# Kernel optimization log

Measured on AMD Instinct MI355X. Metric: run time of the kernel, lower is better.

Reference implementation:

```python
import jax, jax.numpy as jnp
import numpy as np
from jax import lax

STRIDE = 2
PADDING = 2
KERNEL = 5


def _conv_transpose3d(x, weight, bias):
    # weight: [C_in, C_out, kd, kh, kw] (PyTorch ConvTranspose3d layout)
    # Equivalent dense conv: flip kernel spatially, swap in/out channels,
    # lhs_dilation=stride, symmetric padding = dilation*(k-1) - padding.
    w_t = jnp.flip(weight, axis=(2, 3, 4)).transpose(1, 0, 2, 3, 4)  # [C_out, C_in, k,k,k]
    pad = KERNEL - 1 - PADDING  # = 2
    y = lax.conv_general_dilated(
        x, w_t,
        window_strides=(1, 1, 1),
        padding=[(pad, pad)] * 3,
        lhs_dilation=(STRIDE, STRIDE, STRIDE),
        dimension_numbers=("NCDHW", "OIDHW", "NCDHW"),
    )
    return y + bias[None, :, None, None, None]


def _maxpool3d(y, k):
    # PyTorch MaxPool3d(kernel=k) -> stride=k, no padding, floor mode == VALID
    win = (1, 1, k, k, k)
    return lax.reduce_window(y, -jnp.inf, lax.max, win, win, "VALID")


def setup_inputs() -> dict:
    key = jax.random.key(0)
    k1, k2, k3 = jax.random.split(key, 3)
    x = jax.random.normal(k1, (16, 32, 16, 32, 32), dtype=jnp.float32)
    weight = jax.random.normal(k2, (32, 64, 5, 5, 5), dtype=jnp.float32) * 0.05
    bias = jax.random.normal(k3, (64,), dtype=jnp.float32) * 0.05
    return {"x": x, "weight": weight, "bias": bias}


def reference(x, weight, bias):
    y = _conv_transpose3d(x, weight, bias)     # [16, 64, 31, 63, 63]
    y = _maxpool3d(y, 2)                       # [16, 64, 15, 31, 31]
    y = _maxpool3d(y, 3)                       # [16, 64, 5, 10, 10]
    return jnp.sum(y, axis=1, keepdims=True)   # [16, 1, 5, 10, 10]
```

## Files before the change

kernel.cpp:

```cpp
#include <hip/hip_runtime.h>
#include <hip/hip_bf16.h>
#include <math.h>

typedef short bf16x8 __attribute__((ext_vector_type(8)));
typedef float f32x4 __attribute__((ext_vector_type(4)));

constexpr int CIN = 32, COUT = 64, D = 16, H = 32, W = 32;

constexpr size_t WS_XT_OFF = 1u << 20;
constexpr size_t WS_NEED   = WS_XT_OFF + 33554432u;

static __device__ const unsigned char IT_CODE[24] = {
    0, 8, 16, 3,
    1, 9, 17, 11, 19, 7,
    2, 10, 18, 5, 13, 21, 15,
    4, 12, 20, 6, 14, 22, 23};
static __device__ const unsigned char IT_START[5] = {0, 4, 10, 17, 24};
static __device__ const unsigned char EPI_START[10] = {0, 1, 3, 5, 6, 7, 9, 11, 12, 13};
static __device__ const unsigned char EPI_CNT[10]   = {1, 2, 2, 1, 1, 2, 2, 1, 1, 2};

__global__ __launch_bounds__(1024) void prep_all(
    const float* __restrict__ x, const float* __restrict__ w,
    unsigned short* __restrict__ xT, unsigned short* __restrict__ wtp) {
    __shared__ float tile[4][32][33];
    int tid = threadIdx.x;
    if (blockIdx.x < 2048) {
        int sub = tid >> 8, t = tid & 255;
        int tileIdx = blockIdx.x * 4 + sub;
        int ih = tileIdx & 31, id = (tileIdx >> 5) & 15, n = tileIdx >> 9;
        int ci = t >> 3, iwq = t & 7;
        float4 v = ((const float4*)(x + ((((size_t)n * CIN + ci) * D + id) * H + ih) * W))[iwq];
        tile[sub][ci][iwq * 4 + 0] = v.x;
        tile[sub][ci][iwq * 4 + 1] = v.y;
        tile[sub][ci][iwq * 4 + 2] = v.z;
        tile[sub][ci][iwq * 4 + 3] = v.w;
        __syncthreads();
        int iw = t >> 3, ciq = t & 7;
        ushort4 o;
        {
            __hip_bfloat16 b0 = __float2bfloat16(tile[sub][ciq * 4 + 0][iw]);
            __hip_bfloat16 b1 = __float2bfloat16(tile[sub][ciq * 4 + 1][iw]);
            __hip_bfloat16 b2 = __float2bfloat16(tile[sub][ciq * 4 + 2][iw]);
            __hip_bfloat16 b3 = __float2bfloat16(tile[sub][ciq * 4 + 3][iw]);
            o.x = *reinterpret_cast<unsigned short*>(&b0);
            o.y = *reinterpret_cast<unsigned short*>(&b1);
            o.z = *reinterpret_cast<unsigned short*>(&b2);
            o.w = *reinterpret_cast<unsigned short*>(&b3);
        }
        ((ushort4*)(xT + ((((size_t)n * D + id) * H + ih) * W) * 32))[iw * 8 + ciq] = o;
    } else {
        int idx = (blockIdx.x - 2048) * 1024 + tid;
        int ci  = idx & 31;
        int co  = (idx >> 5) & 63;
        int tt  = idx >> 11;
        int t   = tt % 27, cls = tt / 27;
        int td = t / 9, th = (t / 3) % 3, tw = t % 3;
        int pd = (cls >> 2) & 1, ph = (cls >> 1) & 1, pw = cls & 1;
        int kd = pd + 2 * td, kh = ph + 2 * th, kw = pw + 2 * tw;
        float v = 0.f;
        if (kd < 5 && kh < 5 && kw < 5)
            v = w[(ci * COUT + co) * 125 + kd * 25 + kh * 5 + kw];
        __hip_bfloat16 b = __float2bfloat16(v);
        wtp[idx] = *reinterpret_cast<unsigned short*>(&b);
    }
}

__device__ __forceinline__ int lpA(int wrow, int quad) {
    return wrow * 64 + ((quad ^ ((wrow >> 1) & 3)) << 4);
}

__global__ __launch_bounds__(256, 3) void main_k(
    const unsigned short* __restrict__ wtp, const unsigned short* __restrict__ xT,
    const float* __restrict__ bias, float* __restrict__ out)
{
    __shared__ unsigned short Xs[25600];
    int bx = blockIdx.x;
    int h0 = bx % 10;
    int d0 = (bx / 10) % 5;
    int n  = bx / 50;
    int tid = threadIdx.x;

    int id0 = 3 * d0 - 1, ih0 = 3 * h0 - 1;
    for (int i = tid; i < 3200; i += 256) {
        int cb = i & 3, ww = (i >> 2) & 31, hl = (i >> 7) % 5, dd = i / 640;
        int id = id0 + dd, ih = ih0 + hl, iw = ww - 1;
        float4 v = {0.f, 0.f, 0.f, 0.f};
        if (id >= 0 && ih >= 0 && iw >= 0)
            v = ((const float4*)(xT + ((((size_t)n * D + id) * H + ih) * W + iw) * 32))[cb];
        ((float4*)Xs)[(i >> 2) * 4 + (cb ^ ((ww >> 1) & 3))] = v;
    }

    int lane = tid & 63, wv = tid >> 6;
    int l15 = lane & 15, quad = lane >> 4;
    int wv_s = __builtin_amdgcn_readfirstlane(wv);

    int laneB = l15 * 64 + quad * 16;
    int m1 = 16 + l15; if (m1 > 29) m1 = 29;
    int lp00 = lpA(l15 + 0, quad), lp01 = lpA(l15 + 1, quad), lp02 = lpA(l15 + 2, quad);
    int lp10 = lpA(m1 + 0, quad),  lp11 = lpA(m1 + 1, quad),  lp12 = lpA(m1 + 2, quad);

    f32x4 mx[2][4];
#pragma unroll
    for (int mt = 0; mt < 2; ++mt)
#pragma unroll
        for (int nt = 0; nt < 4; ++nt) mx[mt][nt] = (f32x4){-INFINITY, -INFINITY, -INFINITY, -INFINITY};

    __syncthreads();
    const char* xsb = (const char*)Xs;

    int it0 = IT_START[wv_s], it1 = IT_START[wv_s + 1];
#pragma unroll 1
    for (int ii = it0; ii < it1; ++ii) {
        int code  = __builtin_amdgcn_readfirstlane(IT_CODE[ii]);
        int cls   = code & 7;
        int alpha = code >> 3;
        int ntd = 3 - ((cls >> 2) & 1), nth = 3 - ((cls >> 1) & 1), ntw = 3 - (cls & 1);
        const char* tbb = (const char*)wtp + (size_t)cls * 27 * 4096 + laneB;

        f32x4 acc[3][2][4];
#pragma unroll
        for (int b = 0; b < 3; ++b)
#pragma unroll
            for (int mt = 0; mt < 2; ++mt)
#pragma unroll
                for (int nt = 0; nt < 4; ++nt) acc[b][mt][nt] = (f32x4){0.f, 0.f, 0.f, 0.f};

        const int T = ntd * nth * ntw;
        bf16x8 nb0 = *(const bf16x8*)(tbb);
        bf16x8 nb1 = *(const bf16x8*)(tbb + 1024);
        bf16x8 nb2 = *(const bf16x8*)(tbb + 2048);
        bf16x8 nb3 = *(const bf16x8*)(tbb + 3072);
        int ptd = 0, pth = 0, ptw = 0;
        int nQb = ((alpha + 2) * 5 + 2) * 2048;
        int nss = 2;

#pragma unroll 1
        for (int it = 0; it < T; ++it) {
            bf16x8 b0 = nb0, b1 = nb1, b2 = nb2, b3 = nb3;
            const int Qb = nQb, ss = nss;

            if (it + 1 < T) {
                ++ptw;
                if (ptw == ntw) { ptw = 0; ++pth; if (pth == nth) { pth = 0; ++ptd; } }
            }
            nQb = ((alpha + 2 - ptd) * 5 + (2 - pth)) * 2048;
            nss = 2 - ptw;
            const char* bq = tbb + (ptd * 9 + pth * 3 + ptw) * 4096;
            nb0 = *(const bf16x8*)(bq);
            nb1 = *(const bf16x8*)(bq + 1024);
            nb2 = *(const bf16x8*)(bq + 2048);
            nb3 = *(const bf16x8*)(bq + 3072);

            int lpa = ss == 0 ? lp00 : (ss == 1 ? lp01 : lp02);
            int lpb = ss == 0 ? lp10 : (ss == 1 ? lp11 : lp12);

#pragma unroll
            for (int beta = 0; beta < 3; ++beta) {
                const char* rb = xsb + Qb + beta * 2048;
                bf16x8 af0 = *(const bf16x8*)(rb + lpa);
                bf16x8 af1 = *(const bf16x8*)(rb + lpb);
                acc[beta][0][0] = __builtin_amdgcn_mfma_f32_16x16x32_bf16(af0, b0, acc[beta][0][0], 0, 0, 0);
                acc[beta][0][1] = __builtin_amdgcn_mfma_f32_16x16x32_bf16(af0, b1, acc[beta][0][1], 0, 0, 0);
                acc[beta][0][2] = __builtin_amdgcn_mfma_f32_16x16x32_bf16(af0, b2, acc[beta][0][2], 0, 0, 0);
                acc[beta][0][3] = __builtin_amdgcn_mfma_f32_16x16x32_bf16(af0, b3, acc[beta][0][3], 0, 0, 0);
                acc[beta][1][0] = __builtin_amdgcn_mfma_f32_16x16x32_bf16(af1, b0, acc[beta][1][0], 0, 0, 0);
                acc[beta][1][1] = __builtin_amdgcn_mfma_f32_16x16x32_bf16(af1, b1, acc[beta][1][1], 0, 0, 0);
                acc[beta][1][2] = __builtin_amdgcn_mfma_f32_16x16x32_bf16(af1, b2, acc[beta][1][2], 0, 0, 0);
                acc[beta][1][3] = __builtin_amdgcn_mfma_f32_16x16x32_bf16(af1, b3, acc[beta][1][3], 0, 0, 0);
            }
        }

#pragma unroll
        for (int mt = 0; mt < 2; ++mt)
#pragma unroll
            for (int nt = 0; nt < 4; ++nt)
#pragma unroll
                for (int r = 0; r < 4; ++r) {
                    float m = fmaxf(fmaxf(acc[0][mt][nt][r], acc[1][mt][nt][r]), acc[2][mt][nt][r]);
                    mx[mt][nt][r] = fmaxf(mx[mt][nt][r], m);
                }
    }

    __syncthreads();
    float* epi = (float*)Xs;
    int fsm0 = (0x3123 >> (quad * 4)) & 15;
    int fsm1 = (0x4312 >> (quad * 4)) & 15;
#pragma unroll
    for (int mt = 0; mt < 2; ++mt) {
        int fs = mt ? fsm1 : fsm0;
        int g  = mt * 4 + quad;
#pragma unroll
        for (int nt = 0; nt < 4; ++nt) {
            float a0 = mx[mt][nt][0], a1 = mx[mt][nt][1], a2 = mx[mt][nt][2], a3 = mx[mt][nt][3];
            float t01 = fmaxf(a0, a1), t012 = fmaxf(t01, a2), t0123 = fmaxf(t012, a3);
            float pA = fs == 1 ? a0 : (fs == 2 ? t01 : (fs == 3 ? t012 : t0123));
            float t23 = fmaxf(a2, a3), t123 = fmaxf(a1, t23);
            float pB = fs == 1 ? t123 : (fs == 2 ? t23 : (fs == 3 ? a3 : -INFINITY));
            epi[((wv * 8 + g) * 2 + 0) * 64 + nt * 16 + l15] = pA;
            epi[((wv * 8 + g) * 2 + 1) * 64 + nt * 16 + l15] = pB;
        }
    }
    __syncthreads();

    int elemBase = ((n * 5 + d0) * 10 + h0) * 10;
    float bco = bias[lane];
#pragma unroll 1
    for (int win = wv_s; win < 10; win += 4) {
        int st = EPI_START[win], cnt = EPI_CNT[win];
        float v = -INFINITY;
        for (int src = 0; src < 4; ++src)
            for (int e = st; e < st + cnt; ++e)
                v = fmaxf(v, epi[(src * 16 + e) * 64 + lane]);
        v += bco;
#pragma unroll
        for (int off = 32; off > 0; off >>= 1) v += __shfl_xor(v, off);
        if (lane == 0) out[elemBase + win] = v;
    }
}

__global__ __launch_bounds__(256) void fused_fallback(
    const float* __restrict__ x, const float* __restrict__ wsrc,
    const float* __restrict__ bias, float* __restrict__ out)
{
    __shared__ float xs[CIN * 125];
    __shared__ float wmax[4][64];
    const int b  = blockIdx.x;
    const int w0 = b % 10, h0 = (b / 10) % 10, d0 = (b / 100) % 5, n = b / 500;
    const int tid = threadIdx.x;
    const int id0 = 3 * d0 - 1, ih0 = 3 * h0 - 1, iw0 = 3 * w0 - 1;
    for (int e = tid; e < CIN * 125; e += 256) {
        int kk = e % 5, jj = (e / 5) % 5, ii = (e / 25) % 5, c = e / 125;
        int id = id0 + ii, ih = ih0 + jj, iw = iw0 + kk;
        float v = 0.f;
        if (id >= 0 && ih >= 0 && iw >= 0)
            v = x[(((n * CIN + c) * D + id) * H + ih) * W + iw];
        xs[e] = v;
    }
    __syncthreads();
    const int lane = tid & 63, wv = tid >> 6;
    float lmax = -INFINITY;
    for (int ccls = 0; ccls < 2; ++ccls) {
        const int cls = wv * 2 + ccls;
        const int pd = (cls >> 2) & 1, ph = (cls >> 1) & 1, pw = cls & 1;
        float acc[27];
#pragma unroll
        for (int i = 0; i < 27; ++i) acc[i] = 0.f;
        for (int ci = 0; ci < CIN; ++ci) {
            float wr[27];
#pragma unroll
            for (int t = 0; t < 27; ++t) {
                int td = t / 9, th = (t / 3) % 3, tw = t % 3;
                int kd = pd + 2 * td, kh = ph + 2 * th, kw = pw + 2 * tw;
                wr[t] = (kd < 5 && kh < 5 && kw < 5)
                          ? wsrc[((ci * 64 + lane) * 125) + kd * 25 + kh * 5 + kw] : 0.f;
            }
            const float* xb = xs + ci * 125;
#pragma unroll
            for (int td = 0; td < 3; ++td)
#pragma unroll
            for (int th = 0; th < 3; ++th)
#pragma unroll
            for (int tw = 0; tw < 3; ++tw) {
                const float wval = wr[(td * 3 + th) * 3 + tw];
#pragma unroll
                for (int a = 0; a < 3; ++a)
#pragma unroll
                for (int bb = 0; bb < 3; ++bb)
#pragma unroll
                for (int cc = 0; cc < 3; ++cc)
                    acc[(a * 3 + bb) * 3 + cc] +=
                        xb[(a + 2 - td) * 25 + (bb + 2 - th) * 5 + (cc + 2 - tw)] * wval;
            }
        }
#pragma unroll
        for (int i = 0; i < 27; ++i) lmax = fmaxf(lmax, acc[i]);
    }
    wmax[wv][lane] = lmax;
    __syncthreads();
    if (wv == 0) {
        float m = fmaxf(fmaxf(wmax[0][lane], wmax[1][lane]),
                        fmaxf(wmax[2][lane], wmax[3][lane]));
        m += bias[lane];
        for (int off = 32; off > 0; off >>= 1) m += __shfl_down(m, off);
        if (lane == 0) out[b] = m;
    }
}

extern "C" void kernel_launch(void* const* d_in, const int* in_sizes, int n_in,
                              void* d_out, int out_size, void* d_ws, size_t ws_size,
                              hipStream_t stream) {
    const float* x    = (const float*)d_in[0];
    const float* w    = (const float*)d_in[1];
    const float* bias = (const float*)d_in[2];
    float* out = (float*)d_out;

    if (ws_size >= WS_NEED) {
        unsigned short* wtp = (unsigned short*)d_ws;
        unsigned short* xT  = (unsigned short*)((char*)d_ws + WS_XT_OFF);
        prep_all<<<2480, 1024, 0, stream>>>(x, w, xT, wtp);
        main_k<<<800, 256, 0, stream>>>(wtp, xT, bias, out);
    } else {
        fused_fallback<<<8000, 256, 0, stream>>>(x, w, bias, out);
    }
}
```

Before: 212.9 us.

## Split output channels across waves to halve per-wave accumulators and rebalance work

Each wave now computes 32 of the 64 output channels instead of all 64, with the iteration code list doubled to encode a channel-half bit. Waves 0-1 process all parity-class work items for channels 0-31 and waves 2-3 for channels 32-63, replacing the previous uneven split of classes across waves. This halves accumulator registers and B loads per wave, which may raise occupancy and improve load balance. The cost is that each wave re-reads the A fragments from shared memory for twice as many items, and the epilogue buffer layout is changed to combine the two channel halves.

After: 219.6 us. 1.03x slower.

```diff
diff --git a/kernel.cpp b/kernel.cpp
--- a/kernel.cpp
+++ b/kernel.cpp
@@ -10,12 +10,12 @@
 constexpr size_t WS_XT_OFF = 1u << 20;
 constexpr size_t WS_NEED   = WS_XT_OFF + 33554432u;
 
-static __device__ const unsigned char IT_CODE[24] = {
-    0, 8, 16, 3,
-    1, 9, 17, 11, 19, 7,
-    2, 10, 18, 5, 13, 21, 15,
-    4, 12, 20, 6, 14, 22, 23};
-static __device__ const unsigned char IT_START[5] = {0, 4, 10, 17, 24};
+static __device__ const unsigned char IT_CODE[48] = {
+    0, 8, 16, 4, 12, 20, 3, 11, 19, 7,
+    1, 9, 17, 2, 10, 18, 5, 13, 21, 6, 14, 22, 15, 23,
+    32, 40, 48, 36, 44, 52, 35, 43, 51, 39,
+    33, 41, 49, 34, 42, 50, 37, 45, 53, 38, 46, 54, 47, 55};
+static __device__ const unsigned char IT_START[5] = {0, 10, 24, 34, 48};
 static __device__ const unsigned char EPI_START[10] = {0, 1, 3, 5, 6, 7, 9, 11, 12, 13};
 static __device__ const unsigned char EPI_CNT[10]   = {1, 2, 2, 1, 1, 2, 2, 1, 1, 2};
 
@@ -99,11 +99,11 @@
     int lp00 = lpA(l15 + 0, quad), lp01 = lpA(l15 + 1, quad), lp02 = lpA(l15 + 2, quad);
     int lp10 = lpA(m1 + 0, quad),  lp11 = lpA(m1 + 1, quad),  lp12 = lpA(m1 + 2, quad);
 
-    f32x4 mx[2][4];
+    f32x4 mx[2][2];
 #pragma unroll
     for (int mt = 0; mt < 2; ++mt)
 #pragma unroll
-        for (int nt = 0; nt < 4; ++nt) mx[mt][nt] = (f32x4){-INFINITY, -INFINITY, -INFINITY, -INFINITY};
+        for (int nt = 0; nt < 2; ++nt) mx[mt][nt] = (f32x4){-INFINITY, -INFINITY, -INFINITY, -INFINITY};
 
     __syncthreads();
     const char* xsb = (const char*)Xs;
@@ -113,30 +113,29 @@
     for (int ii = it0; ii < it1; ++ii) {
         int code  = __builtin_amdgcn_readfirstlane(IT_CODE[ii]);
         int cls   = code & 7;
-        int alpha = code >> 3;
+        int alpha = (code >> 3) & 3;
+        int coH   = code >> 5;
         int ntd = 3 - ((cls >> 2) & 1), nth = 3 - ((cls >> 1) & 1), ntw = 3 - (cls & 1);
-        const char* tbb = (const char*)wtp + (size_t)cls * 27 * 4096 + laneB;
-
-        f32x4 acc[3][2][4];
+        const char* tbb = (const char*)wtp + (size_t)cls * 27 * 4096 + coH * 2048 + laneB;
+
+        f32x4 acc[3][2][2];
 #pragma unroll
         for (int b = 0; b < 3; ++b)
 #pragma unroll
             for (int mt = 0; mt < 2; ++mt)
 #pragma unroll
-                for (int nt = 0; nt < 4; ++nt) acc[b][mt][nt] = (f32x4){0.f, 0.f, 0.f, 0.f};
+                for (int nt = 0; nt < 2; ++nt) acc[b][mt][nt] = (f32x4){0.f, 0.f, 0.f, 0.f};
 
         const int T = ntd * nth * ntw;
         bf16x8 nb0 = *(const bf16x8*)(tbb);
         bf16x8 nb1 = *(const bf16x8*)(tbb + 1024);
-        bf16x8 nb2 = *(const bf16x8*)(tbb + 2048);
-        bf16x8 nb3 = *(const bf16x8*)(tbb + 3072);
         int ptd = 0, pth = 0, ptw = 0;
         int nQb = ((alpha + 2) * 5 + 2) * 2048;
         int nss = 2;
 
 #pragma unroll 1
         for (int it = 0; it < T; ++it) {
-            bf16x8 b0 = nb0, b1 = nb1, b2 = nb2, b3 = nb3;
+            bf16x8 b0 = nb0, b1 = nb1;
             const int Qb = nQb, ss = nss;
 
             if (it + 1 < T) {
@@ -148,8 +147,6 @@
             const char* bq = tbb + (ptd * 9 + pth * 3 + ptw) * 4096;
             nb0 = *(const bf16x8*)(bq);
             nb1 = *(const bf16x8*)(bq + 1024);
-            nb2 = *(const bf16x8*)(bq + 2048);
-            nb3 = *(const bf16x8*)(bq + 3072);
 
             int lpa = ss == 0 ? lp00 : (ss == 1 ? lp01 : lp02);
             int lpb = ss == 0 ? lp10 : (ss == 1 ? lp11 : lp12);
@@ -161,19 +158,15 @@
                 bf16x8 af1 = *(const bf16x8*)(rb + lpb);
                 acc[beta][0][0] = __builtin_amdgcn_mfma_f32_16x16x32_bf16(af0, b0, acc[beta][0][0], 0, 0, 0);
                 acc[beta][0][1] = __builtin_amdgcn_mfma_f32_16x16x32_bf16(af0, b1, acc[beta][0][1], 0, 0, 0);
-                acc[beta][0][2] = __builtin_amdgcn_mfma_f32_16x16x32_bf16(af0, b2, acc[beta][0][2], 0, 0, 0);
-                acc[beta][0][3] = __builtin_amdgcn_mfma_f32_16x16x32_bf16(af0, b3, acc[beta][0][3], 0, 0, 0);
                 acc[beta][1][0] = __builtin_amdgcn_mfma_f32_16x16x32_bf16(af1, b0, acc[beta][1][0], 0, 0, 0);
                 acc[beta][1][1] = __builtin_amdgcn_mfma_f32_16x16x32_bf16(af1, b1, acc[beta][1][1], 0, 0, 0);
-                acc[beta][1][2] = __builtin_amdgcn_mfma_f32_16x16x32_bf16(af1, b2, acc[beta][1][2], 0, 0, 0);
-                acc[beta][1][3] = __builtin_amdgcn_mfma_f32_16x16x32_bf16(af1, b3, acc[beta][1][3], 0, 0, 0);
             }
         }
 
 #pragma unroll
         for (int mt = 0; mt < 2; ++mt)
 #pragma unroll
-            for (int nt = 0; nt < 4; ++nt)
+            for (int nt = 0; nt < 2; ++nt)
 #pragma unroll
                 for (int r = 0; r < 4; ++r) {
                     float m = fmaxf(fmaxf(acc[0][mt][nt][r], acc[1][mt][nt][r]), acc[2][mt][nt][r]);
@@ -190,27 +183,28 @@
         int fs = mt ? fsm1 : fsm0;
         int g  = mt * 4 + quad;
 #pragma unroll
-        for (int nt = 0; nt < 4; ++nt) {
+        for (int nt = 0; nt < 2; ++nt) {
             float a0 = mx[mt][nt][0], a1 = mx[mt][nt][1], a2 = mx[mt][nt][2], a3 = mx[mt][nt][3];
             float t01 = fmaxf(a0, a1), t012 = fmaxf(t01, a2), t0123 = fmaxf(t012, a3);
             float pA = fs == 1 ? a0 : (fs == 2 ? t01 : (fs == 3 ? t012 : t0123));
             float t23 = fmaxf(a2, a3), t123 = fmaxf(a1, t23);
             float pB = fs == 1 ? t123 : (fs == 2 ? t23 : (fs == 3 ? a3 : -INFINITY));
-            epi[((wv * 8 + g) * 2 + 0) * 64 + nt * 16 + l15] = pA;
-            epi[((wv * 8 + g) * 2 + 1) * 64 + nt * 16 + l15] = pB;
+            epi[(wv * 16 + g * 2 + 0) * 32 + nt * 16 + l15] = pA;
+            epi[(wv * 16 + g * 2 + 1) * 32 + nt * 16 + l15] = pB;
         }
     }
     __syncthreads();
 
     int elemBase = ((n * 5 + d0) * 10 + h0) * 10;
+    int coH = lane >> 5, col = lane & 31;
     float bco = bias[lane];
 #pragma unroll 1
     for (int win = wv_s; win < 10; win += 4) {
         int st = EPI_START[win], cnt = EPI_CNT[win];
         float v = -INFINITY;
-        for (int src = 0; src < 4; ++src)
+        for (int w = 2 * coH; w <= 2 * coH + 1; ++w)
             for (int e = st; e < st + cnt; ++e)
-                v = fmaxf(v, epi[(src * 16 + e) * 64 + lane]);
+                v = fmaxf(v, epi[(w * 16 + e) * 32 + col]);
         v += bco;
 #pragma unroll
         for (int off = 32; off > 0; off >>= 1) v += __shfl_xor(v, off);
```
